# Performance work log

Measured on AMD Instinct MI355X. Metric: run time of the kernel, lower is better.

## Reference

```python
import jax, jax.numpy as jnp
import numpy as np

N_EMBED = 1024
N_HEADS = 16
HEAD = N_EMBED // N_HEADS
EPS = 1e-5


def setup_inputs() -> dict:
    key = jax.random.key(0)
    ks = jax.random.split(key, 16)
    C = N_EMBED
    s = lambda fan_in: 1.0 / np.sqrt(fan_in)
    return {
        "x": jax.random.normal(ks[0], (4, 2048, C), jnp.float32),
        "ln1_g": jnp.ones((C,), jnp.float32),
        "ln1_b": jnp.zeros((C,), jnp.float32),
        "w_attn": jax.random.normal(ks[1], (C, 3 * C), jnp.float32) * s(C),
        "b_attn": jnp.zeros((3 * C,), jnp.float32),
        "w_proj": jax.random.normal(ks[2], (C, C), jnp.float32) * s(C),
        "b_proj": jnp.zeros((C,), jnp.float32),
        "ln2_g": jnp.ones((C,), jnp.float32),
        "ln2_b": jnp.zeros((C,), jnp.float32),
        "w_fc": jax.random.normal(ks[3], (C, 4 * C), jnp.float32) * s(C),
        "b_fc": jnp.zeros((4 * C,), jnp.float32),
        "w_fc2": jax.random.normal(ks[4], (4 * C, C), jnp.float32) * s(4 * C),
        "b_fc2": jnp.zeros((C,), jnp.float32),
    }


def _layernorm(x, g, b):
    mu = jnp.mean(x, axis=-1, keepdims=True)
    var = jnp.mean(jnp.square(x - mu), axis=-1, keepdims=True)
    return (x - mu) * jax.lax.rsqrt(var + EPS) * g + b


def _attention(x, w_attn, b_attn, w_proj, b_proj):
    B, T, C = x.shape
    qkv = x @ w_attn + b_attn  # [B,T,3C]
    q, k, v = jnp.split(qkv, 3, axis=-1)
    q = q.reshape(B, T, N_HEADS, HEAD).transpose(0, 2, 1, 3)  # [B,H,T,D]
    k = k.reshape(B, T, N_HEADS, HEAD).transpose(0, 2, 1, 3)
    v = v.reshape(B, T, N_HEADS, HEAD).transpose(0, 2, 1, 3)
    scale = 1.0 / np.sqrt(HEAD)
    affin = jnp.einsum("bhqd,bhkd->bhqk", q, k) * scale  # [B,H,T,T]
    causal = jnp.tril(jnp.ones((T, T), bool))
    affin = jnp.where(causal, affin, -jnp.inf)
    affin = jax.nn.softmax(affin, axis=-1)
    y = jnp.einsum("bhqk,bhkd->bhqd", affin, v)  # [B,H,T,D]
    y = y.transpose(0, 2, 1, 3).reshape(B, T, C)
    return y @ w_proj + b_proj


def reference(x, ln1_g, ln1_b, w_attn, b_attn, w_proj, b_proj,
              ln2_g, ln2_b, w_fc, b_fc, w_fc2, b_fc2):
    x = x + _attention(_layernorm(x, ln1_g, ln1_b), w_attn, b_attn, w_proj, b_proj)
    h = _layernorm(x, ln2_g, ln2_b)
    h = jax.nn.gelu(h @ w_fc + b_fc, approximate=True)  # tanh GELU
    x = x + (h @ w_fc2 + b_fc2)
    return x
```

## Files before the change

### kernel.cpp

```cpp
#include <hip/hip_runtime.h>
#include <math.h>


#define M_ROWS 8192
#define T_SEQ 2048
#define N_EMB 1024
#define N_HEADS 16
#define HEAD_D 64

typedef _Float16 f16;
typedef __attribute__((ext_vector_type(8))) _Float16 f16x8;
typedef __attribute__((ext_vector_type(4))) _Float16 f16x4;
typedef __attribute__((ext_vector_type(4))) float f32x4;

__device__ __forceinline__ void async16(void* lds, const void* g) {
    __builtin_amdgcn_global_load_lds(
        (const __attribute__((address_space(1))) unsigned int*)g,
        (__attribute__((address_space(3))) unsigned int*)lds, 16, 0, 0);
}

__device__ __forceinline__ float gelu_tanh(float v) {
    float u = 0.7978845608028654f * (v + 0.044715f * v * v * v);
    float e = __expf(2.0f * u);
    float t = 1.0f - 2.0f / (e + 1.0f);
    return 0.5f * v * (1.0f + t);
}

__launch_bounds__(256)
__global__ void wconv_kernel(const float* __restrict__ W, f16* __restrict__ WT,
                             int K, int N) {
    __shared__ float t[32][33];
    int tx = threadIdx.x & 31, ty = threadIdx.x >> 5;
    int n0 = blockIdx.x * 32, k0 = blockIdx.y * 32;
    #pragma unroll
    for (int r = 0; r < 4; r++)
        t[ty * 4 + r][tx] = W[(size_t)(k0 + ty * 4 + r) * N + n0 + tx];
    __syncthreads();
    #pragma unroll
    for (int r = 0; r < 4; r++)
        WT[(size_t)(n0 + ty * 4 + r) * K + k0 + tx] = (f16)t[tx][ty * 4 + r];
}

__launch_bounds__(256)
__global__ void ln_kernel(const float* __restrict__ x, const float* __restrict__ g,
                          const float* __restrict__ b, f16* __restrict__ y) {
    int row = blockIdx.x;
    int tid = threadIdx.x;
    const float* xr = x + (size_t)row * N_EMB;
    float4 v = *(const float4*)(xr + tid * 4);
    float s  = v.x + v.y + v.z + v.w;
    float sq = v.x * v.x + v.y * v.y + v.z * v.z + v.w * v.w;
    #pragma unroll
    for (int off = 32; off > 0; off >>= 1) {
        s  += __shfl_down(s, off);
        sq += __shfl_down(sq, off);
    }
    __shared__ float ws_[4], wq_[4];
    __shared__ float mean_s, rstd_s;
    int lane = tid & 63, wid = tid >> 6;
    if (lane == 0) { ws_[wid] = s; wq_[wid] = sq; }
    __syncthreads();
    if (tid == 0) {
        float st = ws_[0] + ws_[1] + ws_[2] + ws_[3];
        float qt = wq_[0] + wq_[1] + wq_[2] + wq_[3];
        float mu = st * (1.0f / N_EMB);
        float var = qt * (1.0f / N_EMB) - mu * mu;
        mean_s = mu;
        rstd_s = rsqrtf(var + 1e-5f);
    }
    __syncthreads();
    float mu = mean_s, r = rstd_s;
    float4 gv = *(const float4*)(g + tid * 4);
    float4 bv = *(const float4*)(b + tid * 4);
    f16x4 o;
    o.x = (f16)((v.x - mu) * r * gv.x + bv.x);
    o.y = (f16)((v.y - mu) * r * gv.y + bv.y);
    o.z = (f16)((v.z - mu) * r * gv.z + bv.z);
    o.w = (f16)((v.w - mu) * r * gv.w + bv.w);
    *(f16x4*)(y + (size_t)row * N_EMB + tid * 4) = o;
}

template <int EPI>
__launch_bounds__(256)
__global__ void gemm_f16(const f16* __restrict__ A, const f16* __restrict__ Bt,
                         const float* __restrict__ bias, const float* __restrict__ res,
                         float* __restrict__ Cf, f16* __restrict__ Ch,
                         f16* __restrict__ vT, int K, int N) {
    __shared__ f16 As[2][128 * 32];
    __shared__ f16 Bs[2][128 * 32];
    int tid = threadIdx.x;
    int lane = tid & 63, wave = tid >> 6;
    int wr = wave >> 1, wc = wave & 1;
    int quad = lane >> 4, l16 = lane & 15;
    int m0 = blockIdx.y * 128, n0 = blockIdx.x * 128;

    int r0 = tid >> 2;
    int s0 = (tid & 3) * 8;
    const f16* paA0 = A  + (size_t)(m0 + r0) * K + s0;
    const f16* paA1 = A  + (size_t)(m0 + r0 + 64) * K + s0;
    const f16* paB0 = Bt + (size_t)(n0 + r0) * K + s0;
    const f16* paB1 = Bt + (size_t)(n0 + r0 + 64) * K + s0;
    char* dA0 = (char*)As + (size_t)tid * 16;
    char* dA1 = (char*)As + (size_t)(256 + tid) * 16;
    char* dB0 = (char*)Bs + (size_t)tid * 16;
    char* dB1 = (char*)Bs + (size_t)(256 + tid) * 16;

    async16(dA0, paA0);
    async16(dA1, paA1);
    async16(dB0, paB0);
    async16(dB1, paB1);

    f32x4 acc[4][4] = {};
    int p = 0;
    for (int k0 = 0; k0 < K; k0 += 32, p ^= 1) {
        __syncthreads();
        if (k0 + 32 < K) {
            int koff = k0 + 32;
            async16(dA0 + (p ^ 1) * 8192, paA0 + koff);
            async16(dA1 + (p ^ 1) * 8192, paA1 + koff);
            async16(dB0 + (p ^ 1) * 8192, paB0 + koff);
            async16(dB1 + (p ^ 1) * 8192, paB1 + koff);
        }
        const f16* as = As[p];
        const f16* bs = Bs[p];
        f16x8 af[4], bf[4];
        #pragma unroll
        for (int i = 0; i < 4; i++)
            af[i] = *(const f16x8*)&as[(wr * 64 + i * 16 + l16) * 32 + quad * 8];
        #pragma unroll
        for (int j = 0; j < 4; j++)
            bf[j] = *(const f16x8*)&bs[(wc * 64 + j * 16 + l16) * 32 + quad * 8];
        #pragma unroll
        for (int i = 0; i < 4; i++)
            #pragma unroll
            for (int j = 0; j < 4; j++)
                acc[i][j] = __builtin_amdgcn_mfma_f32_16x16x32_f16(
                    af[i], bf[j], acc[i][j], 0, 0, 0);
    }

    #pragma unroll
    for (int i = 0; i < 4; i++) {
        int row0 = m0 + wr * 64 + i * 16 + quad * 4;
        #pragma unroll
        for (int j = 0; j < 4; j++) {
            int col = n0 + wc * 64 + j * 16 + l16;
            float bb = bias[col];
            if (EPI == 3) {
                if (n0 < 2048) {
                    #pragma unroll
                    for (int r = 0; r < 4; r++)
                        Ch[(size_t)(row0 + r) * 2048 + col] = (f16)(acc[i][j][r] + bb);
                } else {
                    int hh = (col - 2048) >> 6, dd = col & 63;
                    int bb_ = row0 >> 11, t0 = row0 & 2047;
                    f16x4 pk;
                    pk.x = (f16)(acc[i][j][0] + bb);
                    pk.y = (f16)(acc[i][j][1] + bb);
                    pk.z = (f16)(acc[i][j][2] + bb);
                    pk.w = (f16)(acc[i][j][3] + bb);
                    *(f16x4*)(vT + ((size_t)(bb_ * 16 + hh) * 64 + dd) * 2048 + t0) = pk;
                }
            } else {
                #pragma unroll
                for (int r = 0; r < 4; r++) {
                    size_t idx = (size_t)(row0 + r) * N + col;
                    float v = acc[i][j][r] + bb;
                    if (EPI == 1) v += res[idx];
                    if (EPI == 2) Ch[idx] = (f16)gelu_tanh(v);
                    else          Cf[idx] = v;
                }
            }
        }
    }
}

__launch_bounds__(256, 2)
__global__ void flash_kernel(const f16* __restrict__ qk, const f16* __restrict__ vT,
                             f16* __restrict__ y) {
    __shared__ __align__(16) char smem[67584];
    f16* Ks = (f16*)smem;
    f16* Vs = (f16*)(smem + 16384);
    int tid = threadIdx.x;
    int lane = tid & 63, w = tid >> 6;
    int quad = lane >> 4, l16 = lane & 15;
    f16* Ps = (f16*)(smem + 32768 + w * 8704);

    int qt = 15 - blockIdx.x;
    int bh = blockIdx.y;
    int b = bh >> 4, h = bh & 15;
    int q0 = qt * 128;

    f16x8 qf[2][2];
    #pragma unroll
    for (int qn = 0; qn < 2; qn++) {
        int q = q0 + w * 32 + qn * 16 + l16;
        #pragma unroll
        for (int dblk = 0; dblk < 2; dblk++) {
            f16x8 t = *(const f16x8*)(qk + (size_t)(b * T_SEQ + q) * 2048 +
                                      h * 64 + dblk * 32 + quad * 8);
            #pragma unroll
            for (int e = 0; e < 8; e++) t[e] = t[e] * (f16)0.125f;
            qf[qn][dblk] = t;
        }
    }

    float m_r[2] = {-INFINITY, -INFINITY};
    float l_r[2] = {0.0f, 0.0f};
    f32x4 Oacc[2][4] = {};

    for (int jt = 0; jt <= qt; jt++) {
        int j0 = jt * 128;
        __syncthreads();
        #pragma unroll
        for (int i = 0; i < 4; i++) {
            int L = i * 256 + tid;
            int j = L >> 3, g1 = L & 7;
            int g = g1 ^ (j & 7);
            async16((char*)Ks + (size_t)L * 16,
                    qk + (size_t)(b * T_SEQ + j0 + j) * 2048 + 1024 + h * 64 + g * 8);
        }
        #pragma unroll
        for (int i = 0; i < 4; i++) {
            int L = i * 256 + tid;
            int d = L >> 4, g1 = L & 15;
            int g = (g1 & 8) | ((g1 ^ d) & 7);
            async16((char*)Vs + (size_t)L * 16,
                    vT + ((size_t)(bh) * 64 + d) * 2048 + j0 + g * 8);
        }
        __syncthreads();

        f32x4 S[8][2];
        #pragma unroll
        for (int jm = 0; jm < 8; jm++) {
            f16x8 kf[2];
            #pragma unroll
            for (int dblk = 0; dblk < 2; dblk++) {
                int j = jm * 16 + l16;
                int g = (dblk * 4 + quad) ^ (j & 7);
                kf[dblk] = *(const f16x8*)(Ks + (size_t)(j * 8 + g) * 8);
            }
            #pragma unroll
            for (int qn = 0; qn < 2; qn++) {
                f32x4 s = {};
                s = __builtin_amdgcn_mfma_f32_16x16x32_f16(kf[0], qf[qn][0], s, 0, 0, 0);
                s = __builtin_amdgcn_mfma_f32_16x16x32_f16(kf[1], qf[qn][1], s, 0, 0, 0);
                S[jm][qn] = s;
            }
        }

        if (jt == qt) {
            #pragma unroll
            for (int jm = 0; jm < 8; jm++)
                #pragma unroll
                for (int qn = 0; qn < 2; qn++)
                    #pragma unroll
                    for (int r = 0; r < 4; r++) {
                        int jl = jm * 16 + quad * 4 + r;
                        int ql = w * 32 + qn * 16 + l16;
                        if (jl > ql) S[jm][qn][r] = -1e30f;
                    }
        }

        float alpha[2];
        #pragma unroll
        for (int qn = 0; qn < 2; qn++) {
            float tmax = -INFINITY;
            #pragma unroll
            for (int jm = 0; jm < 8; jm++)
                #pragma unroll
                for (int r = 0; r < 4; r++)
                    tmax = fmaxf(tmax, S[jm][qn][r]);
            tmax = fmaxf(tmax, __shfl_xor(tmax, 16));
            tmax = fmaxf(tmax, __shfl_xor(tmax, 32));
            float mnew = fmaxf(m_r[qn], tmax);
            alpha[qn] = __expf(m_r[qn] - mnew);
            m_r[qn] = mnew;
            float rsum = 0.0f;
            #pragma unroll
            for (int jm = 0; jm < 8; jm++)
                #pragma unroll
                for (int r = 0; r < 4; r++) {
                    float p = __expf(S[jm][qn][r] - mnew);
                    S[jm][qn][r] = p;
                    rsum += p;
                }
            rsum += __shfl_xor(rsum, 16);
            rsum += __shfl_xor(rsum, 32);
            l_r[qn] = l_r[qn] * alpha[qn] + rsum;
        }

        #pragma unroll
        for (int jm = 0; jm < 8; jm++)
            #pragma unroll
            for (int qn = 0; qn < 2; qn++) {
                f16x4 pk;
                pk.x = (f16)S[jm][qn][0];
                pk.y = (f16)S[jm][qn][1];
                pk.z = (f16)S[jm][qn][2];
                pk.w = (f16)S[jm][qn][3];
                *(f16x4*)(Ps + (size_t)(qn * 16 + l16) * 136 + jm * 16 + quad * 4) = pk;
            }

        float aPV[2][4];
        #pragma unroll
        for (int m = 0; m < 2; m++)
            #pragma unroll
            for (int r = 0; r < 4; r++)
                aPV[m][r] = __shfl(alpha[m], quad * 20 + r);
        #pragma unroll
        for (int m = 0; m < 2; m++)
            #pragma unroll
            for (int n = 0; n < 4; n++)
                #pragma unroll
                for (int r = 0; r < 4; r++)
                    Oacc[m][n][r] *= aPV[m][r];

        #pragma unroll
        for (int kblk = 0; kblk < 4; kblk++) {
            f16x8 pf[2];
            #pragma unroll
            for (int m = 0; m < 2; m++)
                pf[m] = *(const f16x8*)(Ps + (size_t)(m * 16 + l16) * 136 +
                                        kblk * 32 + quad * 8);
            f16x8 vf[4];
            #pragma unroll
            for (int n = 0; n < 4; n++) {
                int d = n * 16 + l16;
                int g = (kblk * 4 + quad);
                int gs = (g & 8) | ((g ^ d) & 7);
                vf[n] = *(const f16x8*)(Vs + (size_t)(d * 16 + gs) * 8);
            }
            #pragma unroll
            for (int m = 0; m < 2; m++)
                #pragma unroll
                for (int n = 0; n < 4; n++)
                    Oacc[m][n] = __builtin_amdgcn_mfma_f32_16x16x32_f16(
                        pf[m], vf[n], Oacc[m][n], 0, 0, 0);
        }
    }

    #pragma unroll
    for (int m = 0; m < 2; m++) {
        float lPV[4];
        #pragma unroll
        for (int r = 0; r < 4; r++)
            lPV[r] = 1.0f / __shfl(l_r[m], quad * 20 + r);
        #pragma unroll
        for (int n = 0; n < 4; n++) {
            #pragma unroll
            for (int r = 0; r < 4; r++) {
                int q = q0 + w * 32 + m * 16 + quad * 4 + r;
                y[(size_t)(b * T_SEQ + q) * N_EMB + h * 64 + n * 16 + l16] =
                    (f16)(Oacc[m][n][r] * lPV[r]);
            }
        }
    }
}

extern "C" void kernel_launch(void* const* d_in, const int* in_sizes, int n_in,
                              void* d_out, int out_size, void* d_ws, size_t ws_size,
                              hipStream_t stream) {
    const float* x      = (const float*)d_in[0];
    const float* ln1_g  = (const float*)d_in[1];
    const float* ln1_b  = (const float*)d_in[2];
    const float* w_attn = (const float*)d_in[3];
    const float* b_attn = (const float*)d_in[4];
    const float* w_proj = (const float*)d_in[5];
    const float* b_proj = (const float*)d_in[6];
    const float* ln2_g  = (const float*)d_in[7];
    const float* ln2_b  = (const float*)d_in[8];
    const float* w_fc   = (const float*)d_in[9];
    const float* b_fc   = (const float*)d_in[10];
    const float* w_fc2  = (const float*)d_in[11];
    const float* b_fc2  = (const float*)d_in[12];
    float* out = (float*)d_out;

    const size_t MB = 1024 * 1024;
    char* ws = (char*)d_ws;
    f16*   lnbuf = (f16*)ws;
    f16*   qkbuf = (f16*)(ws + 16 * MB);
    f16*   vTbuf = (f16*)(ws + 48 * MB);
    f16*   ybuf  = (f16*)(ws + 64 * MB);
    f16*   h     = (f16*)(ws + 80 * MB);
    f16*   wT    = (f16*)(ws + 144 * MB);
    f16* wT_attn = wT;
    f16* wT_proj = wT_attn + (size_t)3072 * 1024;
    f16* wT_fc   = wT_proj + (size_t)1024 * 1024;
    f16* wT_fc2  = wT_fc   + (size_t)1024 * 4096;

    wconv_kernel<<<dim3(3072 / 32, 1024 / 32), 256, 0, stream>>>(w_attn, wT_attn, 1024, 3072);
    wconv_kernel<<<dim3(1024 / 32, 1024 / 32), 256, 0, stream>>>(w_proj, wT_proj, 1024, 1024);
    wconv_kernel<<<dim3(4096 / 32, 1024 / 32), 256, 0, stream>>>(w_fc,   wT_fc,   1024, 4096);
    wconv_kernel<<<dim3(1024 / 32, 4096 / 32), 256, 0, stream>>>(w_fc2,  wT_fc2,  4096, 1024);

    ln_kernel<<<M_ROWS, 256, 0, stream>>>(x, ln1_g, ln1_b, lnbuf);
    gemm_f16<3><<<dim3(3072 / 128, M_ROWS / 128), 256, 0, stream>>>(
        lnbuf, wT_attn, b_attn, nullptr, nullptr, qkbuf, vTbuf, 1024, 3072);
    flash_kernel<<<dim3(16, 64), 256, 0, stream>>>(qkbuf, vTbuf, ybuf);
    gemm_f16<1><<<dim3(1024 / 128, M_ROWS / 128), 256, 0, stream>>>(
        ybuf, wT_proj, b_proj, x, out, nullptr, nullptr, 1024, 1024);
    ln_kernel<<<M_ROWS, 256, 0, stream>>>(out, ln2_g, ln2_b, lnbuf);
    gemm_f16<2><<<dim3(4096 / 128, M_ROWS / 128), 256, 0, stream>>>(
        lnbuf, wT_fc, b_fc, nullptr, nullptr, h, nullptr, 1024, 4096);
    gemm_f16<1><<<dim3(1024 / 128, M_ROWS / 128), 256, 0, stream>>>(
        h, wT_fc2, b_fc2, out, out, nullptr, nullptr, 4096, 1024);
}
```

Before: 576.5 us.

## Double-buffer K in flash attention, use exp2 softmax, add 256-row MLP GEMM

Adds a 512-thread gemm_f16_big kernel with 256x128 tiles and double-buffered async LDS loads, used for the two MLP GEMMs. The flash kernel now prefetches the next K tile into a second buffer while the current tile is processed. It folds log2(e) into the Q scale so the softmax can use exp2f, and halves the per-wave P staging buffer by writing and consuming P in two halves. The aim is to hide global-load latency and enlarge GEMM tiles for more reuse, at the cost of an extra block-wide barrier per tile in attention and unswizzled LDS reads in the new GEMM.

```diff
diff --git a/kernel.cpp b/kernel.cpp
--- a/kernel.cpp
+++ b/kernel.cpp
@@ -174,61 +174,156 @@
     }
 }
 
+template <int EPI>
+__launch_bounds__(512)
+__global__ void gemm_f16_big(const f16* __restrict__ A, const f16* __restrict__ Bt,
+                             const float* __restrict__ bias, const float* __restrict__ res,
+                             float* __restrict__ Cf, f16* __restrict__ Ch,
+                             int K, int N) {
+    __shared__ f16 As[2][256 * 32];
+    __shared__ f16 Bs[2][128 * 32];
+    int tid = threadIdx.x;
+    int lane = tid & 63, wave = tid >> 6;
+    int wr = wave >> 1, wc = wave & 1;
+    int quad = lane >> 4, l16 = lane & 15;
+    int m0 = blockIdx.y * 256, n0 = blockIdx.x * 128;
+
+    int r0 = tid >> 2;
+    int s0 = (tid & 3) * 8;
+    const f16* paA0 = A  + (size_t)(m0 + r0) * K + s0;
+    const f16* paA1 = A  + (size_t)(m0 + r0 + 128) * K + s0;
+    const f16* paB0 = Bt + (size_t)(n0 + r0) * K + s0;
+    char* dA0 = (char*)As + (size_t)tid * 16;
+    char* dA1 = (char*)As + (size_t)(512 + tid) * 16;
+    char* dB0 = (char*)Bs + (size_t)tid * 16;
+
+    async16(dA0, paA0);
+    async16(dA1, paA1);
+    async16(dB0, paB0);
+
+    f32x4 acc[4][4] = {};
+    int p = 0;
+    for (int k0 = 0; k0 < K; k0 += 32, p ^= 1) {
+        __syncthreads();
+        if (k0 + 32 < K) {
+            int koff = k0 + 32;
+            async16(dA0 + (p ^ 1) * 16384, paA0 + koff);
+            async16(dA1 + (p ^ 1) * 16384, paA1 + koff);
+            async16(dB0 + (p ^ 1) * 8192,  paB0 + koff);
+        }
+        const f16* as = As[p];
+        const f16* bs = Bs[p];
+        f16x8 af[4], bf[4];
+        #pragma unroll
+        for (int i = 0; i < 4; i++)
+            af[i] = *(const f16x8*)&as[(wr * 64 + i * 16 + l16) * 32 + quad * 8];
+        #pragma unroll
+        for (int j = 0; j < 4; j++)
+            bf[j] = *(const f16x8*)&bs[(wc * 64 + j * 16 + l16) * 32 + quad * 8];
+        #pragma unroll
+        for (int i = 0; i < 4; i++)
+            #pragma unroll
+            for (int j = 0; j < 4; j++)
+                acc[i][j] = __builtin_amdgcn_mfma_f32_16x16x32_f16(
+                    af[i], bf[j], acc[i][j], 0, 0, 0);
+    }
+
+    #pragma unroll
+    for (int i = 0; i < 4; i++) {
+        int row0 = m0 + wr * 64 + i * 16 + quad * 4;
+        #pragma unroll
+        for (int j = 0; j < 4; j++) {
+            int col = n0 + wc * 64 + j * 16 + l16;
+            float bb = bias[col];
+            #pragma unroll
+            for (int r = 0; r < 4; r++) {
+                size_t idx = (size_t)(row0 + r) * N + col;
+                float v = acc[i][j][r] + bb;
+                if (EPI == 1) v += res[idx];
+                if (EPI == 2) Ch[idx] = (f16)gelu_tanh(v);
+                else          Cf[idx] = v;
+            }
+        }
+    }
+}
+
 __launch_bounds__(256, 2)
 __global__ void flash_kernel(const f16* __restrict__ qk, const f16* __restrict__ vT,
                              f16* __restrict__ y) {
     __shared__ __align__(16) char smem[67584];
-    f16* Ks = (f16*)smem;
-    f16* Vs = (f16*)(smem + 16384);
+    f16* Ks0 = (f16*)smem;
+    f16* Ks1 = (f16*)(smem + 16384);
+    f16* Vs  = (f16*)(smem + 32768);
     int tid = threadIdx.x;
     int lane = tid & 63, w = tid >> 6;
     int quad = lane >> 4, l16 = lane & 15;
-    f16* Ps = (f16*)(smem + 32768 + w * 8704);
+    f16* Ps = (f16*)(smem + 49152 + w * 4608);
 
     int qt = 15 - blockIdx.x;
     int bh = blockIdx.y;
     int b = bh >> 4, h = bh & 15;
     int q0 = qt * 128;
-
+    const size_t qkrow = (size_t)b * T_SEQ * 2048;
+
+    const f16 qsc = (f16)0.1803368801f;
     f16x8 qf[2][2];
     #pragma unroll
     for (int qn = 0; qn < 2; qn++) {
         int q = q0 + w * 32 + qn * 16 + l16;
         #pragma unroll
         for (int dblk = 0; dblk < 2; dblk++) {
-            f16x8 t = *(const f16x8*)(qk + (size_t)(b * T_SEQ + q) * 2048 +
+            f16x8 t = *(const f16x8*)(qk + qkrow + (size_t)q * 2048 +
                                       h * 64 + dblk * 32 + quad * 8);
             #pragma unroll
-            for (int e = 0; e < 8; e++) t[e] = t[e] * (f16)0.125f;
+            for (int e = 0; e < 8; e++) t[e] = t[e] * qsc;
             qf[qn][dblk] = t;
         }
     }
 
-    float m_r[2] = {-INFINITY, -INFINITY};
-    float l_r[2] = {0.0f, 0.0f};
-    f32x4 Oacc[2][4] = {};
-
-    for (int jt = 0; jt <= qt; jt++) {
-        int j0 = jt * 128;
-        __syncthreads();
+    int kj = tid >> 1;
+
+    {
         #pragma unroll
         for (int i = 0; i < 4; i++) {
             int L = i * 256 + tid;
             int j = L >> 3, g1 = L & 7;
             int g = g1 ^ (j & 7);
-            async16((char*)Ks + (size_t)L * 16,
-                    qk + (size_t)(b * T_SEQ + j0 + j) * 2048 + 1024 + h * 64 + g * 8);
-        }
+            async16((char*)Ks0 + (size_t)L * 16,
+                    qk + qkrow + (size_t)j * 2048 + 1024 + h * 64 + g * 8);
+        }
+    }
+
+    float m_r[2] = {-INFINITY, -INFINITY};
+    float l_r[2] = {0.0f, 0.0f};
+    f32x4 Oacc[2][4] = {};
+
+    int p = 0;
+    for (int jt = 0; jt <= qt; jt++, p ^= 1) {
+        int j0 = jt * 128;
+        __syncthreads();
+
         #pragma unroll
         for (int i = 0; i < 4; i++) {
             int L = i * 256 + tid;
             int d = L >> 4, g1 = L & 15;
             int g = (g1 & 8) | ((g1 ^ d) & 7);
             async16((char*)Vs + (size_t)L * 16,
-                    vT + ((size_t)(bh) * 64 + d) * 2048 + j0 + g * 8);
-        }
-        __syncthreads();
-
+                    vT + ((size_t)bh * 64 + d) * 2048 + j0 + g * 8);
+        }
+        if (jt < qt) {
+            char* knext = (char*)(p ? Ks0 : Ks1);
+            int jn0 = j0 + 128;
+            #pragma unroll
+            for (int i = 0; i < 4; i++) {
+                int L = i * 256 + tid;
+                int j = L >> 3, g1 = L & 7;
+                int g = g1 ^ (j & 7);
+                async16(knext + (size_t)L * 16,
+                        qk + qkrow + (size_t)(jn0 + j) * 2048 + 1024 + h * 64 + g * 8);
+            }
+        }
+
+        const f16* kbuf = p ? Ks1 : Ks0;
         f32x4 S[8][2];
         #pragma unroll
         for (int jm = 0; jm < 8; jm++) {
@@ -237,7 +332,7 @@
             for (int dblk = 0; dblk < 2; dblk++) {
                 int j = jm * 16 + l16;
                 int g = (dblk * 4 + quad) ^ (j & 7);
-                kf[dblk] = *(const f16x8*)(Ks + (size_t)(j * 8 + g) * 8);
+                kf[dblk] = *(const f16x8*)(kbuf + (size_t)(j * 8 + g) * 8);
             }
             #pragma unroll
             for (int qn = 0; qn < 2; qn++) {
@@ -273,24 +368,38 @@
             tmax = fmaxf(tmax, __shfl_xor(tmax, 16));
             tmax = fmaxf(tmax, __shfl_xor(tmax, 32));
             float mnew = fmaxf(m_r[qn], tmax);
-            alpha[qn] = __expf(m_r[qn] - mnew);
+            alpha[qn] = exp2f(m_r[qn] - mnew);
             m_r[qn] = mnew;
             float rsum = 0.0f;
             #pragma unroll
             for (int jm = 0; jm < 8; jm++)
                 #pragma unroll
                 for (int r = 0; r < 4; r++) {
-                    float p = __expf(S[jm][qn][r] - mnew);
-                    S[jm][qn][r] = p;
-                    rsum += p;
+                    float pp = exp2f(S[jm][qn][r] - mnew);
+                    S[jm][qn][r] = pp;
+                    rsum += pp;
                 }
             rsum += __shfl_xor(rsum, 16);
             rsum += __shfl_xor(rsum, 32);
             l_r[qn] = l_r[qn] * alpha[qn] + rsum;
         }
 
-        #pragma unroll
-        for (int jm = 0; jm < 8; jm++)
+        float aPV[2][4];
+        #pragma unroll
+        for (int m = 0; m < 2; m++)
+            #pragma unroll
+            for (int r = 0; r < 4; r++)
+                aPV[m][r] = __shfl(alpha[m], quad * 20 + r);
+        #pragma unroll
+        for (int m = 0; m < 2; m++)
+            #pragma unroll
+            for (int n = 0; n < 4; n++)
+                #pragma unroll
+                for (int r = 0; r < 4; r++)
+                    Oacc[m][n][r] *= aPV[m][r];
+
+        #pragma unroll
+        for (int jm = 0; jm < 4; jm++)
             #pragma unroll
             for (int qn = 0; qn < 2; qn++) {
                 f16x4 pk;
@@ -298,35 +407,56 @@
                 pk.y = (f16)S[jm][qn][1];
                 pk.z = (f16)S[jm][qn][2];
                 pk.w = (f16)S[jm][qn][3];
-                *(f16x4*)(Ps + (size_t)(qn * 16 + l16) * 136 + jm * 16 + quad * 4) = pk;
-            }
-
-        float aPV[2][4];
-        #pragma unroll
-        for (int m = 0; m < 2; m++)
-            #pragma unroll
-            for (int r = 0; r < 4; r++)
-                aPV[m][r] = __shfl(alpha[m], quad * 20 + r);
-        #pragma unroll
-        for (int m = 0; m < 2; m++)
-            #pragma unroll
-            for (int n = 0; n < 4; n++)
-                #pragma unroll
-                for (int r = 0; r < 4; r++)
-                    Oacc[m][n][r] *= aPV[m][r];
-
-        #pragma unroll
-        for (int kblk = 0; kblk < 4; kblk++) {
+                *(f16x4*)(Ps + (size_t)(qn * 16 + l16) * 72 + jm * 16 + quad * 4) = pk;
+            }
+
+        __syncthreads();
+
+        #pragma unroll
+        for (int kblk = 0; kblk < 2; kblk++) {
             f16x8 pf[2];
             #pragma unroll
             for (int m = 0; m < 2; m++)
-                pf[m] = *(const f16x8*)(Ps + (size_t)(m * 16 + l16) * 136 +
+                pf[m] = *(const f16x8*)(Ps + (size_t)(m * 16 + l16) * 72 +
                                         kblk * 32 + quad * 8);
             f16x8 vf[4];
             #pragma unroll
             for (int n = 0; n < 4; n++) {
                 int d = n * 16 + l16;
-                int g = (kblk * 4 + quad);
+                int g = kblk * 4 + quad;
+                int gs = (g & 8) | ((g ^ d) & 7);
+                vf[n] = *(const f16x8*)(Vs + (size_t)(d * 16 + gs) * 8);
+            }
+            #pragma unroll
+            for (int m = 0; m < 2; m++)
+                #pragma unroll
+                for (int n = 0; n < 4; n++)
+                    Oacc[m][n] = __builtin_amdgcn_mfma_f32_16x16x32_f16(
+                        pf[m], vf[n], Oacc[m][n], 0, 0, 0);
+        }
+        #pragma unroll
+        for (int jm = 4; jm < 8; jm++)
+            #pragma unroll
+            for (int qn = 0; qn < 2; qn++) {
+                f16x4 pk;
+                pk.x = (f16)S[jm][qn][0];
+                pk.y = (f16)S[jm][qn][1];
+                pk.z = (f16)S[jm][qn][2];
+                pk.w = (f16)S[jm][qn][3];
+                *(f16x4*)(Ps + (size_t)(qn * 16 + l16) * 72 + (jm - 4) * 16 + quad * 4) = pk;
+            }
+        #pragma unroll
+        for (int kblk = 2; kblk < 4; kblk++) {
+            f16x8 pf[2];
+            #pragma unroll
+            for (int m = 0; m < 2; m++)
+                pf[m] = *(const f16x8*)(Ps + (size_t)(m * 16 + l16) * 72 +
+                                        (kblk - 2) * 32 + quad * 8);
+            f16x8 vf[4];
+            #pragma unroll
+            for (int n = 0; n < 4; n++) {
+                int d = n * 16 + l16;
+                int g = kblk * 4 + quad;
                 int gs = (g & 8) | ((g ^ d) & 7);
                 vf[n] = *(const f16x8*)(Vs + (size_t)(d * 16 + gs) * 8);
             }
@@ -400,8 +530,8 @@
     gemm_f16<1><<<dim3(1024 / 128, M_ROWS / 128), 256, 0, stream>>>(
         ybuf, wT_proj, b_proj, x, out, nullptr, nullptr, 1024, 1024);
     ln_kernel<<<M_ROWS, 256, 0, stream>>>(out, ln2_g, ln2_b, lnbuf);
-    gemm_f16<2><<<dim3(4096 / 128, M_ROWS / 128), 256, 0, stream>>>(
-        lnbuf, wT_fc, b_fc, nullptr, nullptr, h, nullptr, 1024, 4096);
-    gemm_f16<1><<<dim3(1024 / 128, M_ROWS / 128), 256, 0, stream>>>(
-        h, wT_fc2, b_fc2, out, out, nullptr, nullptr, 4096, 1024);
-}
+    gemm_f16_big<2><<<dim3(4096 / 128, M_ROWS / 256), 512, 0, stream>>>(
+        lnbuf, wT_fc, b_fc, nullptr, nullptr, h, 1024, 4096);
+    gemm_f16_big<1><<<dim3(1024 / 128, M_ROWS / 256), 512, 0, stream>>>(
+        h, wT_fc2, b_fc2, out, out, nullptr, 4096, 1024);
+}
```

After: 616.2 us. +6.9%, slower.
